# Performance work log

Hardware: AMD Instinct MI355X
Metric: run time of the kernel (lower is better)

The kernel has to match this reference:

```python
import jax, jax.numpy as jnp
import numpy as np


def overlap_and_add(frames, step):
    # frames: [B, F, L] -> [B, (F-1)*step + L] via strided scatter-add
    B, F, L = frames.shape
    out_len = (F - 1) * step + L
    idx = (jnp.arange(F)[:, None] * step + jnp.arange(L)[None, :]).reshape(-1)  # [F*L]
    return jnp.zeros((B, out_len), frames.dtype).at[:, idx].add(frames.reshape(B, F * L))


def setup_inputs() -> dict:
    key = jax.random.key(0)
    k1, k2, k3 = jax.random.split(key, 3)
    bs, frame, basis, spk = 16, 4086, 512, 2
    L = 16  # kernel_size_enc
    speech_length = (frame - 1) * (L // 2) + L  # 32696
    inputs = jax.random.normal(k1, (bs, frame, basis), dtype=jnp.float32)
    estmask = jax.random.uniform(k2, (bs, frame, basis, spk), dtype=jnp.float32)
    W = jax.random.normal(k3, (basis, L), dtype=jnp.float32) * 0.05
    return {"inputs": inputs, "estmask": estmask, "W": W,
            "kernel_size_enc": L, "speech_length": speech_length}


def reference(inputs, estmask, W, kernel_size_enc, speech_length):
    bs, frame, basis = inputs.shape
    spk = estmask.shape[-1]
    # mask-weight: [bs, frame, basis, spk]
    x = inputs[..., None] * estmask
    # -> [bs*spk, frame, basis]
    x = jnp.transpose(x, (0, 3, 1, 2)).reshape(bs * spk, frame, basis)
    # dense projection (no bias, no activation): [bs*spk, frame, L]
    x = jnp.einsum('bfc,cl->bfl', x, W)
    # overlap-and-add with frame_step = L // 2
    x = overlap_and_add(x, kernel_size_enc // 2)  # [bs*spk, samples]
    return x.reshape(bs, spk, speech_length)
```

## Files before the change

### kernel.cpp

```cpp
#include <hip/hip_runtime.h>

constexpr int BS = 16, F = 4086, C = 512, SPK = 2, L = 16, STEP = 8;
constexpr int T    = (F - 1) * STEP + L;
constexpr int ROWS = BS * F;
constexpr int OUT_N = BS * SPK * T;
constexpr int WPAD = 20;
constexpr int WAVES = 4;
constexpr int BLOCK = WAVES * 64;
constexpr int FR  = 4;
constexpr int FPB = WAVES * FR;
constexpr int GRID_A = ROWS / FPB;

template <int CTRL>
__device__ __forceinline__ float dppq(float x) {
    int i = __builtin_bit_cast(int, x);
    i = __builtin_amdgcn_update_dpp(i, i, CTRL, 0xf, 0xf, true);
    return __builtin_bit_cast(float, i);
}
template <int OFF>
__device__ __forceinline__ float swz(float x) {
    int i = __builtin_bit_cast(int, x);
    i = __builtin_amdgcn_ds_swizzle(i, OFF);
    return __builtin_bit_cast(float, i);
}

__device__ __forceinline__ float fold32(float v[32], int lane) {
    const bool h1 = lane & 1, h2 = lane & 2, h4 = lane & 4, h8 = lane & 8, h16 = lane & 16;
#pragma unroll
    for (int i = 0; i < 16; ++i) {
        const float s = h1 ? v[i] : v[i + 16];
        const float k = h1 ? v[i + 16] : v[i];
        v[i] = k + dppq<0xB1>(s);
    }
#pragma unroll
    for (int i = 0; i < 8; ++i) {
        const float s = h2 ? v[i] : v[i + 8];
        const float k = h2 ? v[i + 8] : v[i];
        v[i] = k + dppq<0x4E>(s);
    }
#pragma unroll
    for (int i = 0; i < 4; ++i) {
        const float s = h4 ? v[i] : v[i + 4];
        const float k = h4 ? v[i + 4] : v[i];
        v[i] = k + swz<0x101F>(s);
    }
#pragma unroll
    for (int i = 0; i < 2; ++i) {
        const float s = h8 ? v[i] : v[i + 2];
        const float k = h8 ? v[i + 2] : v[i];
        v[i] = k + swz<0x201F>(s);
    }
    {
        const float s = h16 ? v[0] : v[1];
        const float k = h16 ? v[1] : v[0];
        v[0] = k + swz<0x401F>(s);
    }
    return v[0] + __shfl_xor(v[0], 32, 64);
}

template <bool USE_WS>
__global__ __launch_bounds__(BLOCK, 2) void decoder_proj_kernel(
    const float* __restrict__ inp,
    const float* __restrict__ mask,
    const float* __restrict__ W,
    float* __restrict__ dst)
{
    __shared__ float w_lds[C * WPAD];

    const int tid = threadIdx.x;
    for (int r = tid; r < C; r += BLOCK) {
        const float4* src = reinterpret_cast<const float4*>(W + r * L);
        float4* d = reinterpret_cast<float4*>(w_lds + r * WPAD);
        d[0] = src[0]; d[1] = src[1]; d[2] = src[2]; d[3] = src[3];
    }
    __syncthreads();

    const int wave = tid >> 6, lane = tid & 63;
    const int row0 = blockIdx.x * FPB + wave * FR;

    const int o = ((lane & 1) << 4) | (((lane >> 1) & 1) << 3) | (((lane >> 2) & 1) << 2)
                | (((lane >> 3) & 1) << 1) | ((lane >> 4) & 1);

    float  xiA[8], xiB[8];
    float2 xmA[8], xmB[8];

    auto load = [&](int row, float* xi, float2* xm) {
        const float*  ir = inp + (size_t)row * C;
        const float2* mr = reinterpret_cast<const float2*>(mask) + (size_t)row * C;
#pragma unroll
        for (int i = 0; i < 8; ++i) {
            const int c = lane + 64 * i;
            xi[i] = ir[c];
            xm[i] = mr[c];
        }
    };

    auto compute = [&](const float* xi, const float2* xm) -> float {
        float v[32];
#pragma unroll
        for (int j = 0; j < 32; ++j) v[j] = 0.f;
#pragma unroll
        for (int i = 0; i < 8; ++i) {
            const int c  = lane + 64 * i;
            const float p0 = xi[i] * xm[i].x;
            const float p1 = xi[i] * xm[i].y;
            const float4* wr = reinterpret_cast<const float4*>(&w_lds[c * WPAD]);
#pragma unroll
            for (int q = 0; q < 4; ++q) {
                const float4 wv = wr[q];
                v[4*q+0]    = fmaf(p0, wv.x, v[4*q+0]);
                v[4*q+1]    = fmaf(p0, wv.y, v[4*q+1]);
                v[4*q+2]    = fmaf(p0, wv.z, v[4*q+2]);
                v[4*q+3]    = fmaf(p0, wv.w, v[4*q+3]);
                v[16+4*q+0] = fmaf(p1, wv.x, v[16+4*q+0]);
                v[16+4*q+1] = fmaf(p1, wv.y, v[16+4*q+1]);
                v[16+4*q+2] = fmaf(p1, wv.z, v[16+4*q+2]);
                v[16+4*q+3] = fmaf(p1, wv.w, v[16+4*q+3]);
            }
        }
        return fold32(v, lane);
    };

    auto store = [&](int row, float val) {
        if (USE_WS) {
            if (lane < 32) dst[(size_t)row * 32 + o] = val;
        } else {
            if (lane < 32) {
                const int b = row / F, f = row % F;
                const int s = o >> 4, l = o & 15;
                atomicAdd(&dst[(size_t)(b * SPK + s) * T + f * STEP + l], val);
            }
        }
    };

    load(row0 + 0, xiA, xmA);
    load(row0 + 1, xiB, xmB);
    store(row0 + 0, compute(xiA, xmA));
    load(row0 + 2, xiA, xmA);
    store(row0 + 1, compute(xiB, xmB));
    load(row0 + 3, xiB, xmB);
    store(row0 + 2, compute(xiA, xmA));
    store(row0 + 3, compute(xiB, xmB));
}

__global__ __launch_bounds__(256) void overlap_add_kernel(
    const float* __restrict__ proj,
    float* __restrict__ out)
{
    const int idx = blockIdx.x * blockDim.x + threadIdx.x;
    if (idx >= OUT_N) return;
    const int b = idx / (SPK * T);
    const int r = idx - b * (SPK * T);
    const int s = r / T;
    const int t = r - s * T;
    const int f0 = t >> 3, l0 = t & 7;
    float acc = 0.f;
    if (t < F * STEP) acc += proj[(size_t)(b * F + f0) * 32 + s * 16 + l0];
    if (t >= STEP)    acc += proj[(size_t)(b * F + f0 - 1) * 32 + s * 16 + 8 + l0];
    out[idx] = acc;
}

extern "C" void kernel_launch(void* const* d_in, const int* in_sizes, int n_in,
                              void* d_out, int out_size, void* d_ws, size_t ws_size,
                              hipStream_t stream) {
    const float* inp  = (const float*)d_in[0];
    const float* mask = (const float*)d_in[1];
    const float* W    = (const float*)d_in[2];
    float* out = (float*)d_out;

    const size_t need = (size_t)ROWS * 32 * sizeof(float);
    if (ws_size >= need) {
        float* proj = (float*)d_ws;
        decoder_proj_kernel<true><<<GRID_A, BLOCK, 0, stream>>>(inp, mask, W, proj);
        overlap_add_kernel<<<(OUT_N + 255) / 256, 256, 0, stream>>>(proj, out);
    } else {
        hipMemsetAsync(out, 0, (size_t)OUT_N * sizeof(float), stream);
        decoder_proj_kernel<false><<<GRID_A, BLOCK, 0, stream>>>(inp, mask, W, out);
    }
}
```

Baseline: 86.42 us.

## Pack W as bf16 pairs in LDS, vectorize overlap-add, drop atomic fallback

Weights are stored in LDS as packed bf16 pairs (channel c and c+256 share one 32-bit word), halving LDS footprint and LDS read traffic per FMA. The overlap-add kernel now handles four outputs per thread with 16-byte vector loads and stores. The atomic fallback for a small workspace is removed. Rounding W to bf16 adds numerical error that could fail a tight tolerance, and the vector loads depend on 16-byte alignment of the proj and out offsets.

After: 88.65 us. 2.6% more time.

```diff
diff --git a/kernel.cpp b/kernel.cpp
--- a/kernel.cpp
+++ b/kernel.cpp
@@ -1,15 +1,16 @@
 #include <hip/hip_runtime.h>
 
 constexpr int BS = 16, F = 4086, C = 512, SPK = 2, L = 16, STEP = 8;
-constexpr int T    = (F - 1) * STEP + L;
-constexpr int ROWS = BS * F;
+constexpr int T     = (F - 1) * STEP + L;
+constexpr int ROWS  = BS * F;
 constexpr int OUT_N = BS * SPK * T;
-constexpr int WPAD = 20;
-constexpr int WAVES = 4;
-constexpr int BLOCK = WAVES * 64;
+constexpr int OUT4  = OUT_N / 4;
+constexpr int WAVES = 4, BLOCK = WAVES * 64;
 constexpr int FR  = 4;
 constexpr int FPB = WAVES * FR;
 constexpr int GRID_A = ROWS / FPB;
+
+typedef float f32x4 __attribute__((ext_vector_type(4)));
 
 template <int CTRL>
 __device__ __forceinline__ float dppq(float x) {
@@ -58,20 +59,37 @@
     return v[0] + __shfl_xor(v[0], 32, 64);
 }
 
-template <bool USE_WS>
+__device__ __forceinline__ unsigned pk_bf16(float a, float b) {
+    unsigned ua = __builtin_bit_cast(unsigned, a);
+    unsigned ub = __builtin_bit_cast(unsigned, b);
+    ua += 0x7fffu + ((ua >> 16) & 1u);
+    ub += 0x7fffu + ((ub >> 16) & 1u);
+    return (ua >> 16) | (ub & 0xffff0000u);
+}
+
 __global__ __launch_bounds__(BLOCK, 2) void decoder_proj_kernel(
     const float* __restrict__ inp,
     const float* __restrict__ mask,
     const float* __restrict__ W,
     float* __restrict__ dst)
 {
-    __shared__ float w_lds[C * WPAD];
+    __shared__ uint4 wpk4[4 * 256];
 
     const int tid = threadIdx.x;
-    for (int r = tid; r < C; r += BLOCK) {
-        const float4* src = reinterpret_cast<const float4*>(W + r * L);
-        float4* d = reinterpret_cast<float4*>(w_lds + r * WPAD);
-        d[0] = src[0]; d[1] = src[1]; d[2] = src[2]; d[3] = src[3];
+
+    {
+        const float4* r0 = reinterpret_cast<const float4*>(W + tid * L);
+        const float4* r1 = reinterpret_cast<const float4*>(W + (tid + 256) * L);
+#pragma unroll
+        for (int q = 0; q < 4; ++q) {
+            const float4 a = r0[q], b = r1[q];
+            uint4 d;
+            d.x = pk_bf16(a.x, b.x);
+            d.y = pk_bf16(a.y, b.y);
+            d.z = pk_bf16(a.z, b.z);
+            d.w = pk_bf16(a.w, b.w);
+            wpk4[q * 256 + tid] = d;
+        }
     }
     __syncthreads();
 
@@ -100,37 +118,33 @@
 #pragma unroll
         for (int j = 0; j < 32; ++j) v[j] = 0.f;
 #pragma unroll
-        for (int i = 0; i < 8; ++i) {
-            const int c  = lane + 64 * i;
-            const float p0 = xi[i] * xm[i].x;
-            const float p1 = xi[i] * xm[i].y;
-            const float4* wr = reinterpret_cast<const float4*>(&w_lds[c * WPAD]);
+        for (int i = 0; i < 4; ++i) {
+            const int c2 = lane + 64 * i;
+            const float p0lo = xi[i]     * xm[i].x;
+            const float p1lo = xi[i]     * xm[i].y;
+            const float p0hi = xi[i + 4] * xm[i + 4].x;
+            const float p1hi = xi[i + 4] * xm[i + 4].y;
 #pragma unroll
             for (int q = 0; q < 4; ++q) {
-                const float4 wv = wr[q];
-                v[4*q+0]    = fmaf(p0, wv.x, v[4*q+0]);
-                v[4*q+1]    = fmaf(p0, wv.y, v[4*q+1]);
-                v[4*q+2]    = fmaf(p0, wv.z, v[4*q+2]);
-                v[4*q+3]    = fmaf(p0, wv.w, v[4*q+3]);
-                v[16+4*q+0] = fmaf(p1, wv.x, v[16+4*q+0]);
-                v[16+4*q+1] = fmaf(p1, wv.y, v[16+4*q+1]);
-                v[16+4*q+2] = fmaf(p1, wv.z, v[16+4*q+2]);
-                v[16+4*q+3] = fmaf(p1, wv.w, v[16+4*q+3]);
+                const uint4 wd = wpk4[q * 256 + c2];
+                const unsigned dj[4] = {wd.x, wd.y, wd.z, wd.w};
+#pragma unroll
+                for (int j = 0; j < 4; ++j) {
+                    const int l = 4 * q + j;
+                    const float wlo = __builtin_bit_cast(float, dj[j] << 16);
+                    const float whi = __builtin_bit_cast(float, dj[j] & 0xffff0000u);
+                    v[l]      = fmaf(p0lo, wlo, v[l]);
+                    v[l]      = fmaf(p0hi, whi, v[l]);
+                    v[16 + l] = fmaf(p1lo, wlo, v[16 + l]);
+                    v[16 + l] = fmaf(p1hi, whi, v[16 + l]);
+                }
             }
         }
         return fold32(v, lane);
     };
 
     auto store = [&](int row, float val) {
-        if (USE_WS) {
-            if (lane < 32) dst[(size_t)row * 32 + o] = val;
-        } else {
-            if (lane < 32) {
-                const int b = row / F, f = row % F;
-                const int s = o >> 4, l = o & 15;
-                atomicAdd(&dst[(size_t)(b * SPK + s) * T + f * STEP + l], val);
-            }
-        }
+        if (lane < 32) dst[(size_t)row * 32 + o] = val;
     };
 
     load(row0 + 0, xiA, xmA);
@@ -143,21 +157,26 @@
     store(row0 + 3, compute(xiB, xmB));
 }
 
-__global__ __launch_bounds__(256) void overlap_add_kernel(
+__global__ __launch_bounds__(256) void overlap_add4_kernel(
     const float* __restrict__ proj,
     float* __restrict__ out)
 {
-    const int idx = blockIdx.x * blockDim.x + threadIdx.x;
-    if (idx >= OUT_N) return;
-    const int b = idx / (SPK * T);
-    const int r = idx - b * (SPK * T);
+    const int i4 = blockIdx.x * blockDim.x + threadIdx.x;
+    if (i4 >= OUT4) return;
+    const int t4 = i4 * 4;
+    const int b = t4 / (SPK * T);
+    const int r = t4 - b * (SPK * T);
     const int s = r / T;
     const int t = r - s * T;
     const int f0 = t >> 3, l0 = t & 7;
-    float acc = 0.f;
-    if (t < F * STEP) acc += proj[(size_t)(b * F + f0) * 32 + s * 16 + l0];
-    if (t >= STEP)    acc += proj[(size_t)(b * F + f0 - 1) * 32 + s * 16 + 8 + l0];
-    out[idx] = acc;
+    f32x4 acc = {0.f, 0.f, 0.f, 0.f};
+    if (t < F * STEP)
+        acc = *reinterpret_cast<const f32x4*>(&proj[(size_t)(b * F + f0) * 32 + s * 16 + l0]);
+    if (t >= STEP) {
+        const f32x4 p = *reinterpret_cast<const f32x4*>(&proj[(size_t)(b * F + f0 - 1) * 32 + s * 16 + 8 + l0]);
+        acc += p;
+    }
+    *reinterpret_cast<f32x4*>(&out[t4]) = acc;
 }
 
 extern "C" void kernel_launch(void* const* d_in, const int* in_sizes, int n_in,
@@ -168,13 +187,7 @@
     const float* W    = (const float*)d_in[2];
     float* out = (float*)d_out;
 
-    const size_t need = (size_t)ROWS * 32 * sizeof(float);
-    if (ws_size >= need) {
-        float* proj = (float*)d_ws;
-        decoder_proj_kernel<true><<<GRID_A, BLOCK, 0, stream>>>(inp, mask, W, proj);
-        overlap_add_kernel<<<(OUT_N + 255) / 256, 256, 0, stream>>>(proj, out);
-    } else {
-        hipMemsetAsync(out, 0, (size_t)OUT_N * sizeof(float), stream);
-        decoder_proj_kernel<false><<<GRID_A, BLOCK, 0, stream>>>(inp, mask, W, out);
-    }
+    float* proj = (float*)d_ws;
+    decoder_proj_kernel<<<GRID_A, BLOCK, 0, stream>>>(inp, mask, W, proj);
+    overlap_add4_kernel<<<(OUT4 + 255) / 256, 256, 0, stream>>>(proj, out);
 }
```
